# Kernel optimization log

Measured on AMD Instinct MI355X. Metric: run time of the kernel, lower is better.

The kernel has to match this reference:

```python
import jax, jax.numpy as jnp
import numpy as np

HEAD_SIZE = 32


def setup_inputs() -> dict:
    key = jax.random.key(0)
    ks = jax.random.split(key, 9)
    B, N, M = 2, 512, 512
    Dq = Dk = Dv = 128
    De = 64
    H, O, OUT = 8, HEAD_SIZE, 128
    s = 0.05  # keep logits tame
    return {
        "query": jax.random.normal(ks[0], (B, N, Dq), jnp.float32),
        "key": jax.random.normal(ks[1], (B, M, Dk), jnp.float32),
        "value": jax.random.normal(ks[2], (B, M, Dv), jnp.float32),
        "edge": jax.random.normal(ks[3], (B, N, M, De), jnp.float32),
        "query_kernel": jax.random.normal(ks[4], (H, Dq, O), jnp.float32) * s,
        "key_kernel": jax.random.normal(ks[5], (H, Dk + De, O), jnp.float32) * s,
        "value_kernel": jax.random.normal(ks[6], (H, Dv, O), jnp.float32) * s,
        "projection_kernel": jax.random.normal(ks[7], (H, O, OUT), jnp.float32) * s,
        "projection_bias": jnp.zeros((OUT,), jnp.float32),
    }


def reference(query, key, value, edge, query_kernel, key_kernel,
              value_kernel, projection_kernel, projection_bias):
    # Edge-conditioned keys: concat broadcast key [B,1,M,Dk] with edge [B,N,M,De]
    B, N, _ = query.shape
    M = key.shape[-2]
    key_rep = jnp.broadcast_to(key[..., None, :, :], (B, N, M, key.shape[-1]))
    key_cat = jnp.concatenate([key_rep, edge], axis=-1)           # [B,N,M,Dk+De]
    k = jnp.einsum('bnmi,hio->bnmho', key_cat, key_kernel)        # [B,N,M,H,O]
    q = jnp.einsum('bni,hio->bnho', query, query_kernel)
    q = q / jnp.sqrt(jnp.asarray(HEAD_SIZE, q.dtype))
    v = jnp.einsum('bmi,hio->bmho', value, value_kernel)
    logits = jnp.einsum('bnho,bnmho->bhnm', q, k)                 # [B,H,N,M]
    attn = jax.nn.softmax(logits, axis=-1)
    mh = jnp.einsum('bhnm,bmho->bnho', attn, v)                   # [B,N,H,O]
    out = jnp.einsum('bnhi,hio->bno', mh, projection_kernel)
    out = out + projection_bias
    return out
```

## Files before the change

### kernel.cpp

```cpp
#include <hip/hip_runtime.h>
#include <hip/hip_bf16.h>

#define B_   2
#define N_   512
#define M_   512
#define D_   128
#define DE_  64
#define H_   8
#define O_   32
#define OUT_ 128
#define DKE_ 192
#define MP_  516

typedef unsigned short u16;
typedef unsigned int   u32;
typedef short bf16x8 __attribute__((ext_vector_type(8)));
typedef float floatx4 __attribute__((ext_vector_type(4)));

__device__ __forceinline__ u32 pk2bf(float a, float b) {
    __hip_bfloat162 h = __float22bfloat162_rn(make_float2(a, b));
    return *reinterpret_cast<u32*>(&h);
}
__device__ __forceinline__ u16 f2bf(float a) {
    __hip_bfloat16 h = __float2bfloat16(a);
    return *reinterpret_cast<u16*>(&h);
}
__device__ __forceinline__ float bf2f(u16 x) {
    return __uint_as_float(((u32)x) << 16);
}
__device__ __forceinline__ bf16x8 cvt8(const float4 a, const float4 b) {
    union { u32 u[4]; bf16x8 v; } r;
    r.u[0] = pk2bf(a.x, a.y); r.u[1] = pk2bf(a.z, a.w);
    r.u[2] = pk2bf(b.x, b.y); r.u[3] = pk2bf(b.z, b.w);
    return r.v;
}

__global__ __launch_bounds__(256) void k_proj(
    const float* __restrict__ query, const float* __restrict__ Wq,
    const float* __restrict__ Wk,
    const float* __restrict__ value, const float* __restrict__ Wv,
    u16* __restrict__ qE, u16* __restrict__ vvT)
{
    const int t = threadIdx.x;
    __shared__ float Xs[8][D_];
    __shared__ float qh[8][H_ * O_];

    if (blockIdx.x < 128) {
        const int r0 = blockIdx.x * 8;
        reinterpret_cast<float4*>(&Xs[0][0])[t] =
            reinterpret_cast<const float4*>(query + (size_t)r0 * D_)[t];
        __syncthreads();
        {
            float acc[8] = {0,0,0,0,0,0,0,0};
            const float* wcol = Wq + (t >> 5) * (D_ * O_) + (t & 31);
            for (int k = 0; k < D_; k += 4) {
                const float w0 = wcol[(k+0) * O_];
                const float w1 = wcol[(k+1) * O_];
                const float w2 = wcol[(k+2) * O_];
                const float w3 = wcol[(k+3) * O_];
#pragma unroll
                for (int r = 0; r < 8; ++r) {
                    const float4 x = *reinterpret_cast<const float4*>(&Xs[r][k]);
                    acc[r] += x.x * w0 + x.y * w1 + x.z * w2 + x.w * w3;
                }
            }
#pragma unroll
            for (int r = 0; r < 8; ++r) qh[r][t] = acc[r] * 0.17677669529663687f;
        }
        __syncthreads();

        for (int s = 0; s < 6; ++s) {
            const int hj = t + 256 * s;
            const int h  = hj / DKE_;
            float w[O_];
#pragma unroll
            for (int i = 0; i < O_ / 4; ++i) {
                const float4 x = reinterpret_cast<const float4*>(Wk + (size_t)hj * O_)[i];
                w[4*i] = x.x; w[4*i+1] = x.y; w[4*i+2] = x.z; w[4*i+3] = x.w;
            }
#pragma unroll
            for (int r = 0; r < 8; ++r) {
                const float* qrow = &qh[r][h * O_];
                float a = 0.f;
#pragma unroll
                for (int i = 0; i < O_ / 4; ++i) {
                    const float4 qx = *reinterpret_cast<const float4*>(qrow + 4*i);
                    a += qx.x * w[4*i] + qx.y * w[4*i+1] + qx.z * w[4*i+2] + qx.w * w[4*i+3];
                }
                qE[(size_t)(r0 + r) * (H_ * DKE_) + hj] = f2bf(a);
            }
        }
    } else {
        const int r0 = (blockIdx.x - 128) * 8;
        reinterpret_cast<float4*>(&Xs[0][0])[t] =
            reinterpret_cast<const float4*>(value + (size_t)r0 * D_)[t];
        __syncthreads();

        float acc[8] = {0,0,0,0,0,0,0,0};
        const float* wcol = Wv + (t >> 5) * (D_ * O_) + (t & 31);
        for (int k = 0; k < D_; k += 4) {
            const float w0 = wcol[(k+0) * O_];
            const float w1 = wcol[(k+1) * O_];
            const float w2 = wcol[(k+2) * O_];
            const float w3 = wcol[(k+3) * O_];
#pragma unroll
            for (int r = 0; r < 8; ++r) {
                const float4 x = *reinterpret_cast<const float4*>(&Xs[r][k]);
                acc[r] += x.x * w0 + x.y * w1 + x.z * w2 + x.w * w3;
            }
        }
        const int bb = r0 >> 9, m0 = r0 & 511;
        union { u32 u[4]; uint4 q; } pk;
        pk.u[0] = pk2bf(acc[0], acc[1]);
        pk.u[1] = pk2bf(acc[2], acc[3]);
        pk.u[2] = pk2bf(acc[4], acc[5]);
        pk.u[3] = pk2bf(acc[6], acc[7]);
        *reinterpret_cast<uint4*>(vvT + (size_t)bb * 256 * M_ + (size_t)t * M_ + m0) = pk.q;
    }
}

__global__ __launch_bounds__(256, 4) void k_attn(
    const float* __restrict__ key, const float* __restrict__ edge,
    const u16* __restrict__ qE, const u16* __restrict__ vvT,
    const float* __restrict__ Wp, const float* __restrict__ bias,
    float* __restrict__ out)
{
    const int idx  = blockIdx.x;
    const int b    = idx >> 9;
    const int t    = threadIdx.x;
    const int lane = t & 63;
    const int wv   = t >> 6;

    __shared__ __attribute__((aligned(16))) float attn_s[H_][MP_];
    __shared__ float mh_s[H_ * O_];
    __shared__ float part_s[2][OUT_];

    const int br = lane & 15;
    const int q  = lane >> 4;

    bf16x8 afr[6];
    if (br < 8) {
        const u16* ab = qE + (size_t)idx * (H_ * DKE_) + br * DKE_;
#pragma unroll
        for (int kk = 0; kk < 6; ++kk)
            afr[kk] = *reinterpret_cast<const bf16x8*>(ab + kk * 32 + q * 8);
    } else {
#pragma unroll
        for (int kk = 0; kk < 6; ++kk) afr[kk] = bf16x8{0,0,0,0,0,0,0,0};
    }

    const float* keyb = key  + (size_t)b   * M_ * D_;
    const float* eb   = edge + (size_t)idx * M_ * DE_;

    for (int it = 0; it < 8; ++it) {
        const int tl = it * 4 + wv;
        const int m  = tl * 16 + br;
        const float* kr = keyb + (size_t)m * D_  + q * 8;
        const float* er = eb   + (size_t)m * DE_ + q * 8;
        float4 kf[8], ef[4];
#pragma unroll
        for (int kk = 0; kk < 4; ++kk) {
            kf[2*kk]   = *reinterpret_cast<const float4*>(kr + kk * 32);
            kf[2*kk+1] = *reinterpret_cast<const float4*>(kr + kk * 32 + 4);
        }
#pragma unroll
        for (int kk = 0; kk < 2; ++kk) {
            ef[2*kk]   = *reinterpret_cast<const float4*>(er + kk * 32);
            ef[2*kk+1] = *reinterpret_cast<const float4*>(er + kk * 32 + 4);
        }
        floatx4 acc = {0.f, 0.f, 0.f, 0.f};
#pragma unroll
        for (int kk = 0; kk < 4; ++kk)
            acc = __builtin_amdgcn_mfma_f32_16x16x32_bf16(afr[kk], cvt8(kf[2*kk], kf[2*kk+1]), acc, 0, 0, 0);
#pragma unroll
        for (int kk = 0; kk < 2; ++kk)
            acc = __builtin_amdgcn_mfma_f32_16x16x32_bf16(afr[4+kk], cvt8(ef[2*kk], ef[2*kk+1]), acc, 0, 0, 0);
        if (q < 2) {
#pragma unroll
            for (int i = 0; i < 4; ++i)
                attn_s[q * 4 + i][tl * 16 + br] = acc[i];
        }
    }
    __syncthreads();

    {
        const int h = t >> 5, ml = t & 31;
        float mx = -3.4e38f;
#pragma unroll 2
        for (int j = 0; j < 16; ++j) mx = fmaxf(mx, attn_s[h][ml + 32 * j]);
#pragma unroll
        for (int mask = 16; mask >= 1; mask >>= 1) mx = fmaxf(mx, __shfl_xor(mx, mask, 64));
        float sum = 0.f;
#pragma unroll 2
        for (int j = 0; j < 16; ++j) {
            const int m = ml + 32 * j;
            const float p = __expf(attn_s[h][m] - mx);
            attn_s[h][m] = p;
            sum += p;
        }
#pragma unroll
        for (int mask = 16; mask >= 1; mask >>= 1) sum += __shfl_xor(sum, mask, 64);
        const float inv = 1.f / sum;
#pragma unroll 2
        for (int j = 0; j < 16; ++j) attn_s[h][ml + 32 * j] *= inv;
    }
    __syncthreads();

    {
        const int hh = t >> 5;
        const u16* vrow = vvT + (size_t)b * 256 * M_ + (size_t)t * M_;
        float a0 = 0.f, a1 = 0.f;
        for (int m0 = 0; m0 < M_; m0 += 8) {
            const bf16x8 v8 = *reinterpret_cast<const bf16x8*>(vrow + m0);
            const float4 w0 = *reinterpret_cast<const float4*>(&attn_s[hh][m0]);
            const float4 w1 = *reinterpret_cast<const float4*>(&attn_s[hh][m0 + 4]);
            a0 += w0.x * bf2f((u16)v8[0]) + w0.y * bf2f((u16)v8[1])
                + w0.z * bf2f((u16)v8[2]) + w0.w * bf2f((u16)v8[3]);
            a1 += w1.x * bf2f((u16)v8[4]) + w1.y * bf2f((u16)v8[5])
                + w1.z * bf2f((u16)v8[6]) + w1.w * bf2f((u16)v8[7]);
        }
        mh_s[t] = a0 + a1;
    }
    __syncthreads();

    {
        const int half = t >> 7;
        const int c = t & 127;
        float acc = 0.f;
        const int j0 = half * 128;
#pragma unroll 8
        for (int jj = 0; jj < 128; ++jj)
            acc += mh_s[j0 + jj] * Wp[(size_t)(j0 + jj) * OUT_ + c];
        part_s[half][c] = acc;
    }
    __syncthreads();
    if (t < OUT_)
        out[(size_t)idx * OUT_ + t] = part_s[0][t] + part_s[1][t] + bias[t];
}

extern "C" void kernel_launch(void* const* d_in, const int* in_sizes, int n_in,
                              void* d_out, int out_size, void* d_ws, size_t ws_size,
                              hipStream_t stream)
{
    const float* query = (const float*)d_in[0];
    const float* key   = (const float*)d_in[1];
    const float* value = (const float*)d_in[2];
    const float* edge  = (const float*)d_in[3];
    const float* Wq    = (const float*)d_in[4];
    const float* Wk    = (const float*)d_in[5];
    const float* Wv    = (const float*)d_in[6];
    const float* Wp    = (const float*)d_in[7];
    const float* bias  = (const float*)d_in[8];
    float* out = (float*)d_out;

    u16* qE_ws = (u16*)d_ws;
    u16* vT_ws = (u16*)((char*)d_ws + (size_t)B_*N_*H_*DKE_*2);

    k_proj<<<256,  256, 0, stream>>>(query, Wq, Wk, value, Wv, qE_ws, vT_ws);
    k_attn<<<1024, 256, 0, stream>>>(key, edge, qE_ws, vT_ws, Wp, bias, out);
}
```

Before: 275.4 us.

## Pre-pack key to bf16 MFMA layout, coalesce and prefetch edge via LDS

Adds 64 blocks to the projection kernel that convert key to bf16 in the exact MFMA B-fragment layout, so the attention kernel loads ready fragments instead of reading and converting fp32 key rows in every block. Edge tiles are now read with fully coalesced float4 loads, prefetched one iteration ahead in registers, and rearranged through a double-buffered LDS staging area into fragment order. The value projection is stored in an interleaved layout so that reads in the weighted-sum loop are coalesced across threads. The cost is extra LDS use and more register pressure in the attention kernel.

```diff
diff --git a/kernel.cpp b/kernel.cpp
--- a/kernel.cpp
+++ b/kernel.cpp
@@ -39,7 +39,8 @@
     const float* __restrict__ query, const float* __restrict__ Wq,
     const float* __restrict__ Wk,
     const float* __restrict__ value, const float* __restrict__ Wv,
-    u16* __restrict__ qE, u16* __restrict__ vvT)
+    const float* __restrict__ key,
+    u16* __restrict__ qE, u16* __restrict__ vP, u16* __restrict__ keyF)
 {
     const int t = threadIdx.x;
     __shared__ float Xs[8][D_];
@@ -90,7 +91,7 @@
                 qE[(size_t)(r0 + r) * (H_ * DKE_) + hj] = f2bf(a);
             }
         }
-    } else {
+    } else if (blockIdx.x < 256) {
         const int r0 = (blockIdx.x - 128) * 8;
         reinterpret_cast<float4*>(&Xs[0][0])[t] =
             reinterpret_cast<const float4*>(value + (size_t)r0 * D_)[t];
@@ -115,13 +116,27 @@
         pk.u[1] = pk2bf(acc[2], acc[3]);
         pk.u[2] = pk2bf(acc[4], acc[5]);
         pk.u[3] = pk2bf(acc[6], acc[7]);
-        *reinterpret_cast<uint4*>(vvT + (size_t)bb * 256 * M_ + (size_t)t * M_ + m0) = pk.q;
+        *reinterpret_cast<uint4*>(
+            vP + ((((size_t)bb * 64) + (m0 >> 3)) * 256 + t) * 8) = pk.q;
+    } else {
+        const int kb = blockIdx.x - 256;
+        const int bb = kb >> 5, tl = kb & 31;
+        const int kk = t >> 6, l = t & 63;
+        const int br = l & 15, q = l >> 4;
+        const float* src = key + ((size_t)bb * M_ + tl * 16 + br) * D_ + kk * 32 + q * 8;
+        const float4 f0 = *reinterpret_cast<const float4*>(src);
+        const float4 f1 = *reinterpret_cast<const float4*>(src + 4);
+        union { bf16x8 v; uint4 u; } r;
+        r.v = cvt8(f0, f1);
+        *reinterpret_cast<uint4*>(
+            keyF + ((((size_t)bb * 32 + tl) * 4 + kk) * 64 + l) * 8) = r.u;
     }
 }
 
 __global__ __launch_bounds__(256, 4) void k_attn(
-    const float* __restrict__ key, const float* __restrict__ edge,
-    const u16* __restrict__ qE, const u16* __restrict__ vvT,
+    const float* __restrict__ edge,
+    const u16* __restrict__ qE, const u16* __restrict__ vP,
+    const u16* __restrict__ keyF,
     const float* __restrict__ Wp, const float* __restrict__ bias,
     float* __restrict__ out)
 {
@@ -132,6 +147,7 @@
     const int wv   = t >> 6;
 
     __shared__ __attribute__((aligned(16))) float attn_s[H_][MP_];
+    __shared__ __attribute__((aligned(16))) u16 elds[4][2][2][64][8];
     __shared__ float mh_s[H_ * O_];
     __shared__ float part_s[2][OUT_];
 
@@ -149,32 +165,47 @@
         for (int kk = 0; kk < 6; ++kk) afr[kk] = bf16x8{0,0,0,0,0,0,0,0};
     }
 
-    const float* keyb = key  + (size_t)b   * M_ * D_;
-    const float* eb   = edge + (size_t)idx * M_ * DE_;
-
+    const float* eb  = edge + (size_t)idx * (M_ * DE_);
+    const u16*   kfb = keyF + (size_t)b * (32 * 4 * 64 * 8);
+
+    float4 ef[4];
+    {
+        const float* tb = eb + (size_t)wv * 1024;
+#pragma unroll
+        for (int i = 0; i < 4; ++i)
+            ef[i] = reinterpret_cast<const float4*>(tb)[i * 64 + lane];
+    }
     for (int it = 0; it < 8; ++it) {
-        const int tl = it * 4 + wv;
-        const int m  = tl * 16 + br;
-        const float* kr = keyb + (size_t)m * D_  + q * 8;
-        const float* er = eb   + (size_t)m * DE_ + q * 8;
-        float4 kf[8], ef[4];
+        const int tl  = it * 4 + wv;
+        const int buf = it & 1;
+#pragma unroll
+        for (int i = 0; i < 4; ++i) {
+            const int c    = i * 64 + lane;
+            const int row  = c >> 4, col4 = c & 15;
+            uint2 p;
+            p.x = pk2bf(ef[i].x, ef[i].y);
+            p.y = pk2bf(ef[i].z, ef[i].w);
+            *reinterpret_cast<uint2*>(
+                &elds[wv][buf][col4 >> 3][(((col4 >> 1) & 3) << 4) + row][(col4 & 1) * 4]) = p;
+        }
+        if (it < 7) {
+            const float* tb = eb + (size_t)(tl + 4) * 1024;
+#pragma unroll
+            for (int i = 0; i < 4; ++i)
+                ef[i] = reinterpret_cast<const float4*>(tb)[i * 64 + lane];
+        }
+        floatx4 acc = {0.f, 0.f, 0.f, 0.f};
+        const u16* kf = kfb + (size_t)tl * 4 * 512 + lane * 8;
 #pragma unroll
         for (int kk = 0; kk < 4; ++kk) {
-            kf[2*kk]   = *reinterpret_cast<const float4*>(kr + kk * 32);
-            kf[2*kk+1] = *reinterpret_cast<const float4*>(kr + kk * 32 + 4);
+            const bf16x8 bfr = *reinterpret_cast<const bf16x8*>(kf + kk * 512);
+            acc = __builtin_amdgcn_mfma_f32_16x16x32_bf16(afr[kk], bfr, acc, 0, 0, 0);
         }
 #pragma unroll
         for (int kk = 0; kk < 2; ++kk) {
-            ef[2*kk]   = *reinterpret_cast<const float4*>(er + kk * 32);
-            ef[2*kk+1] = *reinterpret_cast<const float4*>(er + kk * 32 + 4);
-        }
-        floatx4 acc = {0.f, 0.f, 0.f, 0.f};
-#pragma unroll
-        for (int kk = 0; kk < 4; ++kk)
-            acc = __builtin_amdgcn_mfma_f32_16x16x32_bf16(afr[kk], cvt8(kf[2*kk], kf[2*kk+1]), acc, 0, 0, 0);
-#pragma unroll
-        for (int kk = 0; kk < 2; ++kk)
-            acc = __builtin_amdgcn_mfma_f32_16x16x32_bf16(afr[4+kk], cvt8(ef[2*kk], ef[2*kk+1]), acc, 0, 0, 0);
+            const bf16x8 bfr = *reinterpret_cast<const bf16x8*>(&elds[wv][buf][kk][lane][0]);
+            acc = __builtin_amdgcn_mfma_f32_16x16x32_bf16(afr[4 + kk], bfr, acc, 0, 0, 0);
+        }
         if (q < 2) {
 #pragma unroll
             for (int i = 0; i < 4; ++i)
@@ -208,10 +239,11 @@
 
     {
         const int hh = t >> 5;
-        const u16* vrow = vvT + (size_t)b * 256 * M_ + (size_t)t * M_;
+        const u16* vb = vP + (size_t)b * (64 * 256 * 8);
         float a0 = 0.f, a1 = 0.f;
         for (int m0 = 0; m0 < M_; m0 += 8) {
-            const bf16x8 v8 = *reinterpret_cast<const bf16x8*>(vrow + m0);
+            const bf16x8 v8 = *reinterpret_cast<const bf16x8*>(
+                vb + ((size_t)(m0 >> 3) * 256 + t) * 8);
             const float4 w0 = *reinterpret_cast<const float4*>(&attn_s[hh][m0]);
             const float4 w1 = *reinterpret_cast<const float4*>(&attn_s[hh][m0 + 4]);
             a0 += w0.x * bf2f((u16)v8[0]) + w0.y * bf2f((u16)v8[1])
@@ -254,8 +286,9 @@
     float* out = (float*)d_out;
 
     u16* qE_ws = (u16*)d_ws;
-    u16* vT_ws = (u16*)((char*)d_ws + (size_t)B_*N_*H_*DKE_*2);
-
-    k_proj<<<256,  256, 0, stream>>>(query, Wq, Wk, value, Wv, qE_ws, vT_ws);
-    k_attn<<<1024, 256, 0, stream>>>(key, edge, qE_ws, vT_ws, Wp, bias, out);
-}
+    u16* vP_ws = qE_ws + (size_t)B_ * N_ * H_ * DKE_;
+    u16* kF_ws = vP_ws + (size_t)B_ * 64 * 256 * 8;
+
+    k_proj<<<320,  256, 0, stream>>>(query, Wq, Wk, value, Wv, key, qE_ws, vP_ws, kF_ws);
+    k_attn<<<1024, 256, 0, stream>>>(edge, qE_ws, vP_ws, kF_ws, Wp, bias, out);
+}
```

Result: faster. 241.0 us (-12.5%).
